# Optimization experiments

Hardware: AMD Instinct MI355X
Metric: run time of the kernel (lower is better)

The kernel has to match this reference:

```python
import jax, jax.numpy as jnp
import numpy as np

B, S, H, I, E, K = 2, 1024, 768, 1536, 8, 2
CAPACITY_FACTOR = 1.5
ROUTING_TEMP = 1.0
LB_WEIGHT = 0.001


def setup_inputs() -> dict:
    key = jax.random.key(0)
    k_x, k_g, k_w1, k_w3, k_w2 = jax.random.split(key, 5)
    std = 0.02
    return {
        "x": jax.random.normal(k_x, (B, S, H), dtype=jnp.float32),
        "w_gate": jax.random.normal(k_g, (H, E), dtype=jnp.float32) * 0.02,
        "w1": jax.random.normal(k_w1, (E, H, I), dtype=jnp.float32) * std,
        "w3": jax.random.normal(k_w3, (E, H, I), dtype=jnp.float32) * std,
        "w2": jax.random.normal(k_w2, (E, I, H), dtype=jnp.float32) * (std / np.sqrt(2 * 12)),
    }


def _moe_forward(x, w_gate, w1, w3, w2):
    Bb, Ss, Hh = x.shape
    T = Bb * Ss
    xf = x.reshape(T, Hh)

    # --- routing ---
    gate_logits = (xf @ w_gate) / ROUTING_TEMP          # [T, E]
    gate_probs = jax.nn.softmax(gate_logits, axis=-1)   # [T, E]
    topk_probs, topk_idx = jax.lax.top_k(gate_probs, K)  # [T, K]
    topk_probs = topk_probs / (topk_probs.sum(-1, keepdims=True) + 1e-8)

    # --- capacity dropping (per-k slot, token order, like the torch loop) ---
    capacity = max(8, int((T * K // E) * CAPACITY_FACTOR))
    onehot = (topk_idx[:, :, None] == jnp.arange(E)[None, None, :])  # [T, K, E] bool
    ranks = jnp.cumsum(onehot.astype(jnp.int32), axis=0)             # position of token in expert queue
    keep = onehot & (ranks <= capacity)                               # [T, K, E]

    # combine weight per (token, expert): sum over k of kept, clamped routing prob
    w_clamped = jnp.clip(topk_probs, 1e-8, 10.0)                      # [T, K]
    combine = jnp.einsum("tk,tke->te", w_clamped, keep.astype(xf.dtype))  # [T, E]

    # --- dense per-expert SwiGLU (reference form of masked dispatch) ---
    g = jnp.einsum("th,ehi->tei", xf, w1)   # [T, E, I]
    u = jnp.einsum("th,ehi->tei", xf, w3)   # [T, E, I]
    h = jax.nn.silu(g) * u                    # [T, E, I]
    y = jnp.einsum("tei,eih->teh", h, w2)   # [T, E, H]
    out = jnp.einsum("te,teh->th", combine, y).reshape(Bb, Ss, Hh)

    # --- load balancing loss ---
    expert_counts = keep.sum(axis=(0, 1)).astype(jnp.float32)         # [E]
    dropped = (onehot.sum() - keep.sum()).astype(jnp.float32)
    expert_usage = jax.lax.stop_gradient(expert_counts) / float(max(T * K, 1))
    gate_importance = gate_probs.mean(axis=0)                          # [E]
    aux = jnp.sum(expert_usage * gate_importance) * E
    aux = aux + jnp.where(dropped > 0, dropped / float(max(T, 1)) * 0.1, 0.0)
    aux = jnp.minimum(aux, 1.0) * LB_WEIGHT
    return out, aux


def reference(x, w_gate, w1, w3, w2):
    return _moe_forward(x, w_gate, w1, w3, w2)
```

## Files before the change

### kernel.cpp

```cpp
#include <hip/hip_runtime.h>
#include <math.h>

#define T_TOK 2048
#define HD 768
#define ID 1536
#define NE 8
#define CAP 768
#define TK 4096
#define MAXTILES 40

typedef __bf16 bf16_t;
typedef __bf16 bf16x8 __attribute__((ext_vector_type(8)));
typedef float floatx4 __attribute__((ext_vector_type(4)));

__device__ __forceinline__ void gld16(const bf16_t* g, bf16_t* l) {
  __builtin_amdgcn_global_load_lds(
      (__attribute__((address_space(1))) void*)(g),
      (__attribute__((address_space(3))) void*)(l),
      16, 0, 0);
}

__global__ void k_cvt_x(const float* __restrict__ x, bf16_t* __restrict__ xbf,
                        float* __restrict__ imp) {
  int i = blockIdx.x * 256 + threadIdx.x;
  if (blockIdx.x == 0 && threadIdx.x < NE) imp[threadIdx.x] = 0.f;
  const float4* xs = (const float4*)x;
  float4 a = xs[i * 2], b = xs[i * 2 + 1];
  bf16x8 v;
  v[0] = (bf16_t)a.x; v[1] = (bf16_t)a.y; v[2] = (bf16_t)a.z; v[3] = (bf16_t)a.w;
  v[4] = (bf16_t)b.x; v[5] = (bf16_t)b.y; v[6] = (bf16_t)b.z; v[7] = (bf16_t)b.w;
  *(bf16x8*)(xbf + (size_t)i * 8) = v;
}

__global__ void k_route(const float* __restrict__ x, const float* __restrict__ wg,
                        int2* __restrict__ idx2, float2* __restrict__ wc2,
                        float* __restrict__ imp) {
  int t = blockIdx.x;
  int lane = threadIdx.x;
  const float* xr = x + (size_t)t * HD;
  float acc[8] = {0, 0, 0, 0, 0, 0, 0, 0};
  for (int j = 0; j < 12; ++j) {
    int h = j * 64 + lane;
    float xv = xr[h];
    const float4* wr = (const float4*)(wg + (size_t)h * 8);
    float4 w0 = wr[0], w1 = wr[1];
    acc[0] += xv * w0.x; acc[1] += xv * w0.y; acc[2] += xv * w0.z; acc[3] += xv * w0.w;
    acc[4] += xv * w1.x; acc[5] += xv * w1.y; acc[6] += xv * w1.z; acc[7] += xv * w1.w;
  }
#pragma unroll
  for (int e = 0; e < 8; ++e) {
    float v = acc[e];
    for (int s = 1; s < 64; s <<= 1) v += __shfl_xor(v, s, 64);
    acc[e] = v;
  }
  float mx = acc[0];
#pragma unroll
  for (int e = 1; e < 8; ++e) mx = fmaxf(mx, acc[e]);
  float p[8], sum = 0.f;
#pragma unroll
  for (int e = 0; e < 8; ++e) { p[e] = __expf(acc[e] - mx); sum += p[e]; }
#pragma unroll
  for (int e = 0; e < 8; ++e) p[e] /= sum;
  if (lane < 8) atomicAdd(&imp[lane], p[lane]);
  if (lane == 0) {
    int e0 = 0;
#pragma unroll
    for (int e = 1; e < 8; ++e) if (p[e] > p[e0]) e0 = e;
    int e1 = (e0 == 0) ? 1 : 0;
#pragma unroll
    for (int e = 0; e < 8; ++e) if (e != e0 && p[e] > p[e1]) e1 = e;
    float denom = p[e0] + p[e1] + 1e-8f;
    float w0c = fminf(fmaxf(p[e0] / denom, 1e-8f), 10.f);
    float w1c = fminf(fmaxf(p[e1] / denom, 1e-8f), 10.f);
    idx2[t] = make_int2(e0, e1);
    wc2[t] = make_float2(w0c, w1c);
  }
}

__global__ void k_scan(const int2* __restrict__ idx2, const float2* __restrict__ wc2,
                       const float* __restrict__ imp,
                       int* __restrict__ tok_of_row, float* __restrict__ wgt_of_row,
                       int2* __restrict__ tok_rows, int4* __restrict__ tiles,
                       int* __restrict__ meta, float* __restrict__ aux_out) {
  __shared__ int sA[256][16];
  __shared__ int sB[256][8];
  __shared__ int tot8[8];
  int tid = threadIdx.x;
  int t0 = tid * 8;
#pragma unroll
  for (int c = 0; c < 16; ++c) sA[tid][c] = 0;
#pragma unroll
  for (int c = 0; c < 8; ++c) sB[tid][c] = 0;
  for (int j = 0; j < 8; ++j) {
    int t = t0 + j;
    int2 e2 = idx2[t];
    sA[tid][e2.x]++;
    sA[tid][8 + e2.y]++;
    tok_rows[t] = make_int2(-1, -1);
  }
  __syncthreads();
  for (int s = 1; s < 256; s <<= 1) {
    int v[16];
    if (tid >= s) {
#pragma unroll
      for (int c = 0; c < 16; ++c) v[c] = sA[tid - s][c];
    }
    __syncthreads();
    if (tid >= s) {
#pragma unroll
      for (int c = 0; c < 16; ++c) sA[tid][c] += v[c];
    }
    __syncthreads();
  }
  {
    int v[16];
#pragma unroll
    for (int c = 0; c < 16; ++c) v[c] = (tid > 0) ? sA[tid - 1][c] : 0;
    __syncthreads();
#pragma unroll
    for (int c = 0; c < 16; ++c) sA[tid][c] = v[c];
    __syncthreads();
  }
  int keepmask = 0;
  for (int j = 0; j < 8; ++j) {
    int t = t0 + j;
    int2 e2 = idx2[t];
    int r0 = ++sA[tid][e2.x];
    if (r0 <= CAP) { keepmask |= 1 << (j * 2); sB[tid][e2.x]++; }
    int r1 = ++sA[tid][8 + e2.y];
    if (r1 <= CAP) { keepmask |= 1 << (j * 2 + 1); sB[tid][e2.y]++; }
  }
  __syncthreads();
  for (int s = 1; s < 256; s <<= 1) {
    int v[8];
    if (tid >= s) {
#pragma unroll
      for (int c = 0; c < 8; ++c) v[c] = sB[tid - s][c];
    }
    __syncthreads();
    if (tid >= s) {
#pragma unroll
      for (int c = 0; c < 8; ++c) sB[tid][c] += v[c];
    }
    __syncthreads();
  }
  if (tid == 255) {
#pragma unroll
    for (int c = 0; c < 8; ++c) tot8[c] = sB[255][c];
  }
  __syncthreads();
  {
    int v[8];
#pragma unroll
    for (int c = 0; c < 8; ++c) v[c] = (tid > 0) ? sB[tid - 1][c] : 0;
    __syncthreads();
#pragma unroll
    for (int c = 0; c < 8; ++c) sB[tid][c] = v[c];
    __syncthreads();
  }
  int start8[8];
  {
    int run = 0;
#pragma unroll
    for (int c = 0; c < 8; ++c) { start8[c] = run; run += tot8[c]; }
  }
  for (int j = 0; j < 8; ++j) {
    int t = t0 + j;
    int2 e2 = idx2[t];
    float2 wv = wc2[t];
    if (keepmask & (1 << (j * 2))) {
      int pos = sB[tid][e2.x]++;
      int grow = start8[e2.x] + pos;
      tok_of_row[grow] = t; wgt_of_row[grow] = wv.x;
      tok_rows[t].x = grow;
    }
    if (keepmask & (1 << (j * 2 + 1))) {
      int pos = sB[tid][e2.y]++;
      int grow = start8[e2.y] + pos;
      tok_of_row[grow] = t; wgt_of_row[grow] = wv.y;
      tok_rows[t].y = grow;
    }
  }
  __syncthreads();
  if (tid == 0) {
    int numt = 0, totk = 0;
    for (int e = 0; e < NE; ++e) {
      int n = tot8[e]; totk += n; int s = start8[e];
      for (int j = 0; j < n; j += 128) tiles[numt++] = make_int4(e, s + j, min(128, n - j), 0);
    }
    meta[0] = numt;
    int dropped = TK - totk;
    float a = 0.f;
    for (int e = 0; e < NE; ++e)
      a += ((float)tot8[e] / (float)TK) * (imp[e] / (float)T_TOK);
    a *= (float)NE;
    if (dropped > 0) a += (float)dropped / (float)T_TOK * 0.1f;
    a = fminf(a, 1.f) * 0.001f;
    aux_out[0] = a;
  }
}

__global__ void k_tr(const float* __restrict__ src, bf16_t* __restrict__ dst,
                     int R, int C) {
  __shared__ bf16_t tl[64][65];
  int e = blockIdx.z;
  int r0 = blockIdx.y * 64, c0 = blockIdx.x * 64;
  int tid = threadIdx.x;
  int lr = tid >> 2, lc = (tid & 3) * 16;
  const float* s = src + ((size_t)e * R + (r0 + lr)) * C + c0 + lc;
#pragma unroll
  for (int j = 0; j < 16; j += 4) {
    float4 v = *(const float4*)(s + j);
    tl[lr][lc + j + 0] = (bf16_t)v.x;
    tl[lr][lc + j + 1] = (bf16_t)v.y;
    tl[lr][lc + j + 2] = (bf16_t)v.z;
    tl[lr][lc + j + 3] = (bf16_t)v.w;
  }
  __syncthreads();
  int oc = tid >> 2, orr = (tid & 3) * 16;
  bf16_t* d = dst + ((size_t)e * C + (c0 + oc)) * R + r0 + orr;
  bf16x8 v0, v1;
#pragma unroll
  for (int j = 0; j < 8; ++j) v0[j] = tl[orr + j][oc];
#pragma unroll
  for (int j = 0; j < 8; ++j) v1[j] = tl[orr + 8 + j][oc];
  *(bf16x8*)d = v0;
  *(bf16x8*)(d + 8) = v1;
}

__global__ __launch_bounds__(256, 2)
void k_gemm1(const bf16_t* __restrict__ xbf, const bf16_t* __restrict__ w1t,
             const bf16_t* __restrict__ w3t, const int* __restrict__ tok_of_row,
             const int4* __restrict__ tiles, const int* __restrict__ meta,
             bf16_t* __restrict__ h_ws) {
  int numt = meta[0];
  int bx = blockIdx.x;
  if (bx >= numt) return;
  int4 tlr = tiles[bx];
  int e = tlr.x, grow0 = tlr.y, nrows = tlr.z;
  int cy = blockIdx.y;

  __shared__ __attribute__((aligned(16))) bf16_t Abuf[128 * 32];
  __shared__ __attribute__((aligned(16))) bf16_t B1buf[128 * 32];
  __shared__ __attribute__((aligned(16))) bf16_t B3buf[128 * 32];

  int tid = threadIdx.x;
  int lane = tid & 63, wv = tid >> 6;
  int wm = wv & 1, wn = wv >> 1;
  int lr = lane & 15, q = lane >> 4;
  int rdc = (q ^ ((lane >> 1) & 3)) * 8;
  int srow = lane >> 2;
  int gch = ((lane & 3) ^ ((lane >> 3) & 3)) * 8;

  int ra = wv * 32 + srow;
  int tokA0 = tok_of_row[grow0 + min(ra, nrows - 1)];
  int tokA1 = tok_of_row[grow0 + min(ra + 16, nrows - 1)];
  const bf16_t* gA0 = xbf + (size_t)tokA0 * HD + gch;
  const bf16_t* gA1 = xbf + (size_t)tokA1 * HD + gch;
  int nb = cy * 128 + wv * 32 + srow;
  const bf16_t* gB1a = w1t + ((size_t)e * ID + nb) * HD + gch;
  const bf16_t* gB1b = gB1a + (size_t)16 * HD;
  const bf16_t* gB3a = w3t + ((size_t)e * ID + nb) * HD + gch;
  const bf16_t* gB3b = gB3a + (size_t)16 * HD;
  bf16_t* lA0 = &Abuf[(wv * 32) * 32];
  bf16_t* lA1 = &Abuf[(wv * 32 + 16) * 32];
  bf16_t* lB1a = &B1buf[(wv * 32) * 32];
  bf16_t* lB1b = &B1buf[(wv * 32 + 16) * 32];
  bf16_t* lB3a = &B3buf[(wv * 32) * 32];
  bf16_t* lB3b = &B3buf[(wv * 32 + 16) * 32];

  floatx4 accg[4][4] = {};
  floatx4 accu[4][4] = {};

  for (int kk = 0; kk < 24; ++kk) {
    __syncthreads();
    gld16(gA0, lA0);  gld16(gA1, lA1);
    gld16(gB1a, lB1a); gld16(gB1b, lB1b);
    gld16(gB3a, lB3a); gld16(gB3b, lB3b);
    gA0 += 32; gA1 += 32; gB1a += 32; gB1b += 32; gB3a += 32; gB3b += 32;
    __syncthreads();
    bf16x8 af[4], b1f[4], b3f[4];
#pragma unroll
    for (int i = 0; i < 4; ++i) af[i] = *(const bf16x8*)&Abuf[(wm * 64 + i * 16 + lr) * 32 + rdc];
#pragma unroll
    for (int i = 0; i < 4; ++i) b1f[i] = *(const bf16x8*)&B1buf[(wn * 64 + i * 16 + lr) * 32 + rdc];
#pragma unroll
    for (int i = 0; i < 4; ++i) b3f[i] = *(const bf16x8*)&B3buf[(wn * 64 + i * 16 + lr) * 32 + rdc];
#pragma unroll
    for (int i = 0; i < 4; ++i)
#pragma unroll
      for (int j = 0; j < 4; ++j) {
        accg[i][j] = __builtin_amdgcn_mfma_f32_16x16x32_bf16(af[i], b1f[j], accg[i][j], 0, 0, 0);
        accu[i][j] = __builtin_amdgcn_mfma_f32_16x16x32_bf16(af[i], b3f[j], accu[i][j], 0, 0, 0);
      }
  }
#pragma unroll
  for (int i = 0; i < 4; ++i)
#pragma unroll
    for (int r = 0; r < 4; ++r) {
      int rl = wm * 64 + i * 16 + q * 4 + r;
      if (rl < nrows) {
        size_t rb = (size_t)(grow0 + rl) * ID + cy * 128 + wn * 64 + lr;
#pragma unroll
        for (int j = 0; j < 4; ++j) {
          float gg = accg[i][j][r], uu = accu[i][j][r];
          float sg = gg / (1.f + __expf(-gg));
          h_ws[rb + j * 16] = (bf16_t)(sg * uu);
        }
      }
    }
}

__global__ __launch_bounds__(256, 2)
void k_gemm2(const bf16_t* __restrict__ h_ws, const bf16_t* __restrict__ w2t,
             const int4* __restrict__ tiles, const int* __restrict__ meta,
             float* __restrict__ y_ws) {
  int numt = meta[0];
  int bx = blockIdx.x;
  if (bx >= numt) return;
  int4 tlr = tiles[bx];
  int e = tlr.x, grow0 = tlr.y, nrows = tlr.z;
  int cy = blockIdx.y;

  __shared__ __attribute__((aligned(16))) bf16_t Abuf[128 * 32];
  __shared__ __attribute__((aligned(16))) bf16_t Bbuf[128 * 32];

  int tid = threadIdx.x;
  int lane = tid & 63, wv = tid >> 6;
  int wm = wv & 1, wn = wv >> 1;
  int lr = lane & 15, q = lane >> 4;
  int rdc = (q ^ ((lane >> 1) & 3)) * 8;
  int srow = lane >> 2;
  int gch = ((lane & 3) ^ ((lane >> 3) & 3)) * 8;

  int ra = wv * 32 + srow;
  const bf16_t* gA0 = h_ws + (size_t)(grow0 + min(ra, nrows - 1)) * ID + gch;
  const bf16_t* gA1 = h_ws + (size_t)(grow0 + min(ra + 16, nrows - 1)) * ID + gch;
  int nb = cy * 128 + wv * 32 + srow;
  const bf16_t* gB0 = w2t + ((size_t)e * HD + nb) * ID + gch;
  const bf16_t* gB1 = gB0 + (size_t)16 * ID;
  bf16_t* lA0 = &Abuf[(wv * 32) * 32];
  bf16_t* lA1 = &Abuf[(wv * 32 + 16) * 32];
  bf16_t* lB0 = &Bbuf[(wv * 32) * 32];
  bf16_t* lB1 = &Bbuf[(wv * 32 + 16) * 32];

  floatx4 acc[4][4] = {};

  for (int kk = 0; kk < 48; ++kk) {
    __syncthreads();
    gld16(gA0, lA0); gld16(gA1, lA1);
    gld16(gB0, lB0); gld16(gB1, lB1);
    gA0 += 32; gA1 += 32; gB0 += 32; gB1 += 32;
    __syncthreads();
    bf16x8 af[4], bfr[4];
#pragma unroll
    for (int i = 0; i < 4; ++i) af[i] = *(const bf16x8*)&Abuf[(wm * 64 + i * 16 + lr) * 32 + rdc];
#pragma unroll
    for (int i = 0; i < 4; ++i) bfr[i] = *(const bf16x8*)&Bbuf[(wn * 64 + i * 16 + lr) * 32 + rdc];
#pragma unroll
    for (int i = 0; i < 4; ++i)
#pragma unroll
      for (int j = 0; j < 4; ++j)
        acc[i][j] = __builtin_amdgcn_mfma_f32_16x16x32_bf16(af[i], bfr[j], acc[i][j], 0, 0, 0);
  }
#pragma unroll
  for (int i = 0; i < 4; ++i)
#pragma unroll
    for (int r = 0; r < 4; ++r) {
      int rl = wm * 64 + i * 16 + q * 4 + r;
      if (rl < nrows) {
        size_t rb = (size_t)(grow0 + rl) * HD + cy * 128 + wn * 64 + lr;
#pragma unroll
        for (int j = 0; j < 4; ++j) y_ws[rb + j * 16] = acc[i][j][r];
      }
    }
}

__global__ void k_comb(const float* __restrict__ y_ws, const int2* __restrict__ tok_rows,
                       const float* __restrict__ wgt_of_row, float* __restrict__ out) {
  int idx = blockIdx.x * 256 + threadIdx.x;
  int t = idx / 192;
  int c = idx - t * 192;
  int2 rr = tok_rows[t];
  float vx = 0.f, vy = 0.f, vz = 0.f, vw = 0.f;
  if (rr.x >= 0) {
    float w = wgt_of_row[rr.x];
    float4 a = *(const float4*)(y_ws + (size_t)rr.x * HD + c * 4);
    vx += w * a.x; vy += w * a.y; vz += w * a.z; vw += w * a.w;
  }
  if (rr.y >= 0) {
    float w = wgt_of_row[rr.y];
    float4 a = *(const float4*)(y_ws + (size_t)rr.y * HD + c * 4);
    vx += w * a.x; vy += w * a.y; vz += w * a.z; vw += w * a.w;
  }
  float4 v = make_float4(vx, vy, vz, vw);
  *(float4*)(out + (size_t)t * HD + c * 4) = v;
}

extern "C" void kernel_launch(void* const* d_in, const int* in_sizes, int n_in,
                              void* d_out, int out_size, void* d_ws, size_t ws_size,
                              hipStream_t stream) {
  const float* x  = (const float*)d_in[0];
  const float* wg = (const float*)d_in[1];
  const float* w1 = (const float*)d_in[2];
  const float* w3 = (const float*)d_in[3];
  const float* w2 = (const float*)d_in[4];
  float* out = (float*)d_out;

  char* ws = (char*)d_ws;
  bf16_t* xbf  = (bf16_t*)(ws + 0);
  bf16_t* w1t  = (bf16_t*)(ws + 3145728);
  bf16_t* w3t  = (bf16_t*)(ws + 22020096);
  bf16_t* w2t  = (bf16_t*)(ws + 40894464);
  bf16_t* h_ws = (bf16_t*)(ws + 59768832);
  float*  y_ws = (float*)(ws + 72351744);
  int2*   idx2 = (int2*)(ws + 84934656);
  float2* wc2  = (float2*)(ws + 84951040);
  int*    tok_of_row = (int*)(ws + 84967424);
  float*  wgt_of_row = (float*)(ws + 84983808);
  int2*   tok_rows   = (int2*)(ws + 85000192);
  int4*   tiles      = (int4*)(ws + 85016576);
  int*    meta       = (int*)(ws + 85017600);
  float*  imp        = (float*)(ws + 85017856);

  float* aux_out = out + (size_t)T_TOK * HD;

  k_cvt_x<<<768, 256, 0, stream>>>(x, xbf, imp);
  k_route<<<T_TOK, 64, 0, stream>>>(x, wg, idx2, wc2, imp);
  k_scan<<<1, 256, 0, stream>>>(idx2, wc2, imp, tok_of_row, wgt_of_row,
                                tok_rows, tiles, meta, aux_out);
  k_tr<<<dim3(24, 12, 8), 256, 0, stream>>>(w1, w1t, HD, ID);
  k_tr<<<dim3(24, 12, 8), 256, 0, stream>>>(w3, w3t, HD, ID);
  k_tr<<<dim3(12, 24, 8), 256, 0, stream>>>(w2, w2t, ID, HD);
  k_gemm1<<<dim3(MAXTILES, 12), 256, 0, stream>>>(xbf, w1t, w3t, tok_of_row,
                                                  tiles, meta, h_ws);
  k_gemm2<<<dim3(MAXTILES, 6), 256, 0, stream>>>(h_ws, w2t, tiles, meta, y_ws);
  k_comb<<<1536, 256, 0, stream>>>(y_ws, tok_rows, wgt_of_row, out);
}
```

Measured before the change: 285.6 us.

## Fuse routing/convert, simplify scan, merge transposes, shrink GEMM tiles, atomic combine

Folds the x-to-bf16 conversion into the routing kernel and replaces the two-pass per-thread prefix scan with a warp-shuffle scan per (slot, expert) wave. The three weight transpose launches become one, and the tile list is replaced by a fixed per-expert grid. Both GEMMs narrow their N tile from 128 to 64 with higher occupancy hints to launch more blocks. The combine kernel and the y workspace are removed: gemm2 scales its results and atomically adds them into a zeroed output. This cuts launches and a round trip through global memory, at the cost of float atomics, nondeterministic summation order and more A-tile reloads.

```diff
diff --git a/kernel.cpp b/kernel.cpp
--- a/kernel.cpp
+++ b/kernel.cpp
@@ -7,10 +7,10 @@
 #define NE 8
 #define CAP 768
 #define TK 4096
-#define MAXTILES 40
 
 typedef __bf16 bf16_t;
 typedef __bf16 bf16x8 __attribute__((ext_vector_type(8)));
+typedef __bf16 bf16x4 __attribute__((ext_vector_type(4)));
 typedef float floatx4 __attribute__((ext_vector_type(4)));
 
 __device__ __forceinline__ void gld16(const bf16_t* g, bf16_t* l) {
@@ -20,32 +20,32 @@
       16, 0, 0);
 }
 
-__global__ void k_cvt_x(const float* __restrict__ x, bf16_t* __restrict__ xbf,
+__global__ void k_route(const float* __restrict__ x, const float* __restrict__ wg,
+                        bf16_t* __restrict__ xbf, int2* __restrict__ idx2,
+                        float2* __restrict__ wc2, int2* __restrict__ tok_rows,
                         float* __restrict__ imp) {
-  int i = blockIdx.x * 256 + threadIdx.x;
-  if (blockIdx.x == 0 && threadIdx.x < NE) imp[threadIdx.x] = 0.f;
-  const float4* xs = (const float4*)x;
-  float4 a = xs[i * 2], b = xs[i * 2 + 1];
-  bf16x8 v;
-  v[0] = (bf16_t)a.x; v[1] = (bf16_t)a.y; v[2] = (bf16_t)a.z; v[3] = (bf16_t)a.w;
-  v[4] = (bf16_t)b.x; v[5] = (bf16_t)b.y; v[6] = (bf16_t)b.z; v[7] = (bf16_t)b.w;
-  *(bf16x8*)(xbf + (size_t)i * 8) = v;
-}
-
-__global__ void k_route(const float* __restrict__ x, const float* __restrict__ wg,
-                        int2* __restrict__ idx2, float2* __restrict__ wc2,
-                        float* __restrict__ imp) {
-  int t = blockIdx.x;
-  int lane = threadIdx.x;
+  int t = blockIdx.x * 4 + (threadIdx.x >> 6);
+  int lane = threadIdx.x & 63;
   const float* xr = x + (size_t)t * HD;
+  int off = lane * 12;
+  float4 a = *(const float4*)(xr + off);
+  float4 b = *(const float4*)(xr + off + 4);
+  float4 c = *(const float4*)(xr + off + 8);
+  float xv[12] = {a.x, a.y, a.z, a.w, b.x, b.y, b.z, b.w, c.x, c.y, c.z, c.w};
+  bf16x4 s0, s1, s2;
+#pragma unroll
+  for (int j = 0; j < 4; ++j) { s0[j] = (bf16_t)xv[j]; s1[j] = (bf16_t)xv[4 + j]; s2[j] = (bf16_t)xv[8 + j]; }
+  bf16_t* xo = xbf + (size_t)t * HD + off;
+  *(bf16x4*)xo = s0; *(bf16x4*)(xo + 4) = s1; *(bf16x4*)(xo + 8) = s2;
+
   float acc[8] = {0, 0, 0, 0, 0, 0, 0, 0};
-  for (int j = 0; j < 12; ++j) {
-    int h = j * 64 + lane;
-    float xv = xr[h];
-    const float4* wr = (const float4*)(wg + (size_t)h * 8);
+#pragma unroll
+  for (int jj = 0; jj < 12; ++jj) {
+    const float4* wr = (const float4*)(wg + (size_t)(off + jj) * 8);
     float4 w0 = wr[0], w1 = wr[1];
-    acc[0] += xv * w0.x; acc[1] += xv * w0.y; acc[2] += xv * w0.z; acc[3] += xv * w0.w;
-    acc[4] += xv * w1.x; acc[5] += xv * w1.y; acc[6] += xv * w1.z; acc[7] += xv * w1.w;
+    float v = xv[jj];
+    acc[0] += v * w0.x; acc[1] += v * w0.y; acc[2] += v * w0.z; acc[3] += v * w0.w;
+    acc[4] += v * w1.x; acc[5] += v * w1.y; acc[6] += v * w1.z; acc[7] += v * w1.w;
   }
 #pragma unroll
   for (int e = 0; e < 8; ++e) {
@@ -74,143 +74,92 @@
     float w1c = fminf(fmaxf(p[e1] / denom, 1e-8f), 10.f);
     idx2[t] = make_int2(e0, e1);
     wc2[t] = make_float2(w0c, w1c);
+    tok_rows[t] = make_int2(-1, -1);
   }
 }
 
 __global__ void k_scan(const int2* __restrict__ idx2, const float2* __restrict__ wc2,
                        const float* __restrict__ imp,
                        int* __restrict__ tok_of_row, float* __restrict__ wgt_of_row,
-                       int2* __restrict__ tok_rows, int4* __restrict__ tiles,
-                       int* __restrict__ meta, float* __restrict__ aux_out) {
-  __shared__ int sA[256][16];
-  __shared__ int sB[256][8];
-  __shared__ int tot8[8];
+                       int2* __restrict__ tok_rows, int2* __restrict__ cnt_start,
+                       float* __restrict__ aux_out) {
+  __shared__ int sTot[16];
+  __shared__ int sPos[8];
   int tid = threadIdx.x;
-  int t0 = tid * 8;
-#pragma unroll
-  for (int c = 0; c < 16; ++c) sA[tid][c] = 0;
-#pragma unroll
-  for (int c = 0; c < 8; ++c) sB[tid][c] = 0;
-  for (int j = 0; j < 8; ++j) {
-    int t = t0 + j;
-    int2 e2 = idx2[t];
-    sA[tid][e2.x]++;
-    sA[tid][8 + e2.y]++;
-    tok_rows[t] = make_int2(-1, -1);
-  }
-  __syncthreads();
-  for (int s = 1; s < 256; s <<= 1) {
-    int v[16];
-    if (tid >= s) {
-#pragma unroll
-      for (int c = 0; c < 16; ++c) v[c] = sA[tid - s][c];
-    }
-    __syncthreads();
-    if (tid >= s) {
-#pragma unroll
-      for (int c = 0; c < 16; ++c) sA[tid][c] += v[c];
-    }
-    __syncthreads();
-  }
-  {
-    int v[16];
-#pragma unroll
-    for (int c = 0; c < 16; ++c) v[c] = (tid > 0) ? sA[tid - 1][c] : 0;
-    __syncthreads();
-#pragma unroll
-    for (int c = 0; c < 16; ++c) sA[tid][c] = v[c];
-    __syncthreads();
-  }
-  int keepmask = 0;
-  for (int j = 0; j < 8; ++j) {
-    int t = t0 + j;
-    int2 e2 = idx2[t];
-    int r0 = ++sA[tid][e2.x];
-    if (r0 <= CAP) { keepmask |= 1 << (j * 2); sB[tid][e2.x]++; }
-    int r1 = ++sA[tid][8 + e2.y];
-    if (r1 <= CAP) { keepmask |= 1 << (j * 2 + 1); sB[tid][e2.y]++; }
-  }
-  __syncthreads();
-  for (int s = 1; s < 256; s <<= 1) {
-    int v[8];
-    if (tid >= s) {
-#pragma unroll
-      for (int c = 0; c < 8; ++c) v[c] = sB[tid - s][c];
-    }
-    __syncthreads();
-    if (tid >= s) {
-#pragma unroll
-      for (int c = 0; c < 8; ++c) sB[tid][c] += v[c];
-    }
-    __syncthreads();
-  }
-  if (tid == 255) {
-#pragma unroll
-    for (int c = 0; c < 8; ++c) tot8[c] = sB[255][c];
-  }
-  __syncthreads();
-  {
-    int v[8];
-#pragma unroll
-    for (int c = 0; c < 8; ++c) v[c] = (tid > 0) ? sB[tid - 1][c] : 0;
-    __syncthreads();
-#pragma unroll
-    for (int c = 0; c < 8; ++c) sB[tid][c] = v[c];
-    __syncthreads();
-  }
-  int start8[8];
-  {
-    int run = 0;
-#pragma unroll
-    for (int c = 0; c < 8; ++c) { start8[c] = run; run += tot8[c]; }
-  }
-  for (int j = 0; j < 8; ++j) {
-    int t = t0 + j;
-    int2 e2 = idx2[t];
-    float2 wv = wc2[t];
-    if (keepmask & (1 << (j * 2))) {
-      int pos = sB[tid][e2.x]++;
-      int grow = start8[e2.x] + pos;
-      tok_of_row[grow] = t; wgt_of_row[grow] = wv.x;
-      tok_rows[t].x = grow;
-    }
-    if (keepmask & (1 << (j * 2 + 1))) {
-      int pos = sB[tid][e2.y]++;
-      int grow = start8[e2.y] + pos;
-      tok_of_row[grow] = t; wgt_of_row[grow] = wv.y;
-      tok_rows[t].y = grow;
-    }
-  }
+  int w = tid >> 6, lane = tid & 63;
+  int s = w >> 3, e = w & 7;
+  int t0 = lane * 32;
+  int cnt = 0;
+  for (int j = 0; j < 32; ++j) {
+    int2 p = idx2[t0 + j];
+    int ex = s ? p.y : p.x;
+    cnt += (ex == e) ? 1 : 0;
+  }
+  int incl = cnt;
+  for (int d = 1; d < 64; d <<= 1) {
+    int v = __shfl_up(incl, d, 64);
+    if (lane >= d) incl += v;
+  }
+  int excl = incl - cnt;
+  if (lane == 63) sTot[w] = incl;
   __syncthreads();
   if (tid == 0) {
-    int numt = 0, totk = 0;
-    for (int e = 0; e < NE; ++e) {
-      int n = tot8[e]; totk += n; int s = start8[e];
-      for (int j = 0; j < n; j += 128) tiles[numt++] = make_int4(e, s + j, min(128, n - j), 0);
+    int run = 0;
+    float a = 0.f;
+    for (int ee = 0; ee < 8; ++ee) {
+      int k = min(sTot[ee], CAP) + min(sTot[8 + ee], CAP);
+      sPos[ee] = run;
+      cnt_start[ee] = make_int2(run, k);
+      a += ((float)k / (float)TK) * (imp[ee] / (float)T_TOK);
+      run += k;
     }
-    meta[0] = numt;
-    int dropped = TK - totk;
-    float a = 0.f;
-    for (int e = 0; e < NE; ++e)
-      a += ((float)tot8[e] / (float)TK) * (imp[e] / (float)T_TOK);
     a *= (float)NE;
+    int dropped = TK - run;
     if (dropped > 0) a += (float)dropped / (float)T_TOK * 0.1f;
     a = fminf(a, 1.f) * 0.001f;
     aux_out[0] = a;
   }
-}
-
-__global__ void k_tr(const float* __restrict__ src, bf16_t* __restrict__ dst,
-                     int R, int C) {
+  __syncthreads();
+  int rank = excl;
+  for (int j = 0; j < 32; ++j) {
+    int t = t0 + j;
+    int2 p = idx2[t];
+    int ex = s ? p.y : p.x;
+    if (ex == e) {
+      rank++;
+      if (rank <= CAP) {
+        int pos = atomicAdd(&sPos[e], 1);
+        tok_of_row[pos] = t;
+        float2 wv = wc2[t];
+        wgt_of_row[pos] = s ? wv.y : wv.x;
+        ((int*)tok_rows)[2 * t + s] = pos;
+      }
+    }
+  }
+}
+
+__global__ void k_tr(const float* __restrict__ w1, const float* __restrict__ w3,
+                     const float* __restrict__ w2, bf16_t* __restrict__ w1t,
+                     bf16_t* __restrict__ w3t, bf16_t* __restrict__ w2t) {
   __shared__ bf16_t tl[64][65];
-  int e = blockIdx.z;
-  int r0 = blockIdx.y * 64, c0 = blockIdx.x * 64;
+  int z = blockIdx.z;
+  const float* src; bf16_t* dst; int R, C, r0, c0;
+  if (z < 16) {
+    R = HD; C = ID; r0 = blockIdx.y * 64; c0 = blockIdx.x * 64;
+    int e = z & 7;
+    if (z < 8) { src = w1 + (size_t)e * R * C; dst = w1t + (size_t)e * R * C; }
+    else       { src = w3 + (size_t)e * R * C; dst = w3t + (size_t)e * R * C; }
+  } else {
+    R = ID; C = HD; r0 = blockIdx.x * 64; c0 = blockIdx.y * 64;
+    int e = z - 16;
+    src = w2 + (size_t)e * R * C; dst = w2t + (size_t)e * R * C;
+  }
   int tid = threadIdx.x;
   int lr = tid >> 2, lc = (tid & 3) * 16;
-  const float* s = src + ((size_t)e * R + (r0 + lr)) * C + c0 + lc;
+  const float* sp = src + (size_t)(r0 + lr) * C + c0 + lc;
 #pragma unroll
   for (int j = 0; j < 16; j += 4) {
-    float4 v = *(const float4*)(s + j);
+    float4 v = *(const float4*)(sp + j);
     tl[lr][lc + j + 0] = (bf16_t)v.x;
     tl[lr][lc + j + 1] = (bf16_t)v.y;
     tl[lr][lc + j + 2] = (bf16_t)v.z;
@@ -218,7 +167,7 @@
   }
   __syncthreads();
   int oc = tid >> 2, orr = (tid & 3) * 16;
-  bf16_t* d = dst + ((size_t)e * C + (c0 + oc)) * R + r0 + orr;
+  bf16_t* d = dst + (size_t)(c0 + oc) * R + r0 + orr;
   bf16x8 v0, v1;
 #pragma unroll
   for (int j = 0; j < 8; ++j) v0[j] = tl[orr + j][oc];
@@ -228,21 +177,21 @@
   *(bf16x8*)(d + 8) = v1;
 }
 
-__global__ __launch_bounds__(256, 2)
+__global__ __launch_bounds__(256, 3)
 void k_gemm1(const bf16_t* __restrict__ xbf, const bf16_t* __restrict__ w1t,
              const bf16_t* __restrict__ w3t, const int* __restrict__ tok_of_row,
-             const int4* __restrict__ tiles, const int* __restrict__ meta,
-             bf16_t* __restrict__ h_ws) {
-  int numt = meta[0];
-  int bx = blockIdx.x;
-  if (bx >= numt) return;
-  int4 tlr = tiles[bx];
-  int e = tlr.x, grow0 = tlr.y, nrows = tlr.z;
+             const int2* __restrict__ cnt_start, bf16_t* __restrict__ h_ws) {
+  int e = blockIdx.x & 7, j = blockIdx.x >> 3;
+  int2 cs = cnt_start[e];
+  int nrows = cs.y - j * 128;
+  if (nrows <= 0) return;
+  if (nrows > 128) nrows = 128;
+  int grow0 = cs.x + j * 128;
   int cy = blockIdx.y;
 
   __shared__ __attribute__((aligned(16))) bf16_t Abuf[128 * 32];
-  __shared__ __attribute__((aligned(16))) bf16_t B1buf[128 * 32];
-  __shared__ __attribute__((aligned(16))) bf16_t B3buf[128 * 32];
+  __shared__ __attribute__((aligned(16))) bf16_t B1buf[64 * 32];
+  __shared__ __attribute__((aligned(16))) bf16_t B3buf[64 * 32];
 
   int tid = threadIdx.x;
   int lane = tid & 63, wv = tid >> 6;
@@ -257,41 +206,36 @@
   int tokA1 = tok_of_row[grow0 + min(ra + 16, nrows - 1)];
   const bf16_t* gA0 = xbf + (size_t)tokA0 * HD + gch;
   const bf16_t* gA1 = xbf + (size_t)tokA1 * HD + gch;
-  int nb = cy * 128 + wv * 32 + srow;
-  const bf16_t* gB1a = w1t + ((size_t)e * ID + nb) * HD + gch;
-  const bf16_t* gB1b = gB1a + (size_t)16 * HD;
-  const bf16_t* gB3a = w3t + ((size_t)e * ID + nb) * HD + gch;
-  const bf16_t* gB3b = gB3a + (size_t)16 * HD;
+  int nb = cy * 64 + wv * 16 + srow;
+  const bf16_t* gB1 = w1t + ((size_t)e * ID + nb) * HD + gch;
+  const bf16_t* gB3 = w3t + ((size_t)e * ID + nb) * HD + gch;
   bf16_t* lA0 = &Abuf[(wv * 32) * 32];
   bf16_t* lA1 = &Abuf[(wv * 32 + 16) * 32];
-  bf16_t* lB1a = &B1buf[(wv * 32) * 32];
-  bf16_t* lB1b = &B1buf[(wv * 32 + 16) * 32];
-  bf16_t* lB3a = &B3buf[(wv * 32) * 32];
-  bf16_t* lB3b = &B3buf[(wv * 32 + 16) * 32];
-
-  floatx4 accg[4][4] = {};
-  floatx4 accu[4][4] = {};
+  bf16_t* lB1 = &B1buf[(wv * 16) * 32];
+  bf16_t* lB3 = &B3buf[(wv * 16) * 32];
+
+  floatx4 accg[4][2] = {};
+  floatx4 accu[4][2] = {};
 
   for (int kk = 0; kk < 24; ++kk) {
     __syncthreads();
-    gld16(gA0, lA0);  gld16(gA1, lA1);
-    gld16(gB1a, lB1a); gld16(gB1b, lB1b);
-    gld16(gB3a, lB3a); gld16(gB3b, lB3b);
-    gA0 += 32; gA1 += 32; gB1a += 32; gB1b += 32; gB3a += 32; gB3b += 32;
+    gld16(gA0, lA0); gld16(gA1, lA1);
+    gld16(gB1, lB1); gld16(gB3, lB3);
+    gA0 += 32; gA1 += 32; gB1 += 32; gB3 += 32;
     __syncthreads();
-    bf16x8 af[4], b1f[4], b3f[4];
+    bf16x8 af[4], b1f[2], b3f[2];
 #pragma unroll
     for (int i = 0; i < 4; ++i) af[i] = *(const bf16x8*)&Abuf[(wm * 64 + i * 16 + lr) * 32 + rdc];
 #pragma unroll
-    for (int i = 0; i < 4; ++i) b1f[i] = *(const bf16x8*)&B1buf[(wn * 64 + i * 16 + lr) * 32 + rdc];
-#pragma unroll
-    for (int i = 0; i < 4; ++i) b3f[i] = *(const bf16x8*)&B3buf[(wn * 64 + i * 16 + lr) * 32 + rdc];
+    for (int i = 0; i < 2; ++i) b1f[i] = *(const bf16x8*)&B1buf[(wn * 32 + i * 16 + lr) * 32 + rdc];
+#pragma unroll
+    for (int i = 0; i < 2; ++i) b3f[i] = *(const bf16x8*)&B3buf[(wn * 32 + i * 16 + lr) * 32 + rdc];
 #pragma unroll
     for (int i = 0; i < 4; ++i)
 #pragma unroll
-      for (int j = 0; j < 4; ++j) {
-        accg[i][j] = __builtin_amdgcn_mfma_f32_16x16x32_bf16(af[i], b1f[j], accg[i][j], 0, 0, 0);
-        accu[i][j] = __builtin_amdgcn_mfma_f32_16x16x32_bf16(af[i], b3f[j], accu[i][j], 0, 0, 0);
+      for (int jj = 0; jj < 2; ++jj) {
+        accg[i][jj] = __builtin_amdgcn_mfma_f32_16x16x32_bf16(af[i], b1f[jj], accg[i][jj], 0, 0, 0);
+        accu[i][jj] = __builtin_amdgcn_mfma_f32_16x16x32_bf16(af[i], b3f[jj], accu[i][jj], 0, 0, 0);
       }
   }
 #pragma unroll
@@ -300,30 +244,31 @@
     for (int r = 0; r < 4; ++r) {
       int rl = wm * 64 + i * 16 + q * 4 + r;
       if (rl < nrows) {
-        size_t rb = (size_t)(grow0 + rl) * ID + cy * 128 + wn * 64 + lr;
-#pragma unroll
-        for (int j = 0; j < 4; ++j) {
-          float gg = accg[i][j][r], uu = accu[i][j][r];
+        size_t rb = (size_t)(grow0 + rl) * ID + cy * 64 + wn * 32 + lr;
+#pragma unroll
+        for (int jj = 0; jj < 2; ++jj) {
+          float gg = accg[i][jj][r], uu = accu[i][jj][r];
           float sg = gg / (1.f + __expf(-gg));
-          h_ws[rb + j * 16] = (bf16_t)(sg * uu);
+          h_ws[rb + jj * 16] = (bf16_t)(sg * uu);
         }
       }
     }
 }
 
-__global__ __launch_bounds__(256, 2)
+__global__ __launch_bounds__(256, 4)
 void k_gemm2(const bf16_t* __restrict__ h_ws, const bf16_t* __restrict__ w2t,
-             const int4* __restrict__ tiles, const int* __restrict__ meta,
-             float* __restrict__ y_ws) {
-  int numt = meta[0];
-  int bx = blockIdx.x;
-  if (bx >= numt) return;
-  int4 tlr = tiles[bx];
-  int e = tlr.x, grow0 = tlr.y, nrows = tlr.z;
+             const int* __restrict__ tok_of_row, const float* __restrict__ wgt_of_row,
+             const int2* __restrict__ cnt_start, float* __restrict__ out) {
+  int e = blockIdx.x & 7, j = blockIdx.x >> 3;
+  int2 cs = cnt_start[e];
+  int nrows = cs.y - j * 128;
+  if (nrows <= 0) return;
+  if (nrows > 128) nrows = 128;
+  int grow0 = cs.x + j * 128;
   int cy = blockIdx.y;
 
   __shared__ __attribute__((aligned(16))) bf16_t Abuf[128 * 32];
-  __shared__ __attribute__((aligned(16))) bf16_t Bbuf[128 * 32];
+  __shared__ __attribute__((aligned(16))) bf16_t Bbuf[64 * 32];
 
   int tid = threadIdx.x;
   int lane = tid & 63, wv = tid >> 6;
@@ -336,32 +281,30 @@
   int ra = wv * 32 + srow;
   const bf16_t* gA0 = h_ws + (size_t)(grow0 + min(ra, nrows - 1)) * ID + gch;
   const bf16_t* gA1 = h_ws + (size_t)(grow0 + min(ra + 16, nrows - 1)) * ID + gch;
-  int nb = cy * 128 + wv * 32 + srow;
-  const bf16_t* gB0 = w2t + ((size_t)e * HD + nb) * ID + gch;
-  const bf16_t* gB1 = gB0 + (size_t)16 * ID;
+  int nb = cy * 64 + wv * 16 + srow;
+  const bf16_t* gB = w2t + ((size_t)e * HD + nb) * ID + gch;
   bf16_t* lA0 = &Abuf[(wv * 32) * 32];
   bf16_t* lA1 = &Abuf[(wv * 32 + 16) * 32];
-  bf16_t* lB0 = &Bbuf[(wv * 32) * 32];
-  bf16_t* lB1 = &Bbuf[(wv * 32 + 16) * 32];
-
-  floatx4 acc[4][4] = {};
+  bf16_t* lB = &Bbuf[(wv * 16) * 32];
+
+  floatx4 acc[4][2] = {};
 
   for (int kk = 0; kk < 48; ++kk) {
     __syncthreads();
     gld16(gA0, lA0); gld16(gA1, lA1);
-    gld16(gB0, lB0); gld16(gB1, lB1);
-    gA0 += 32; gA1 += 32; gB0 += 32; gB1 += 32;
+    gld16(gB, lB);
+    gA0 += 32; gA1 += 32; gB += 32;
     __syncthreads();
-    bf16x8 af[4], bfr[4];
+    bf16x8 af[4], bfr[2];
 #pragma unroll
     for (int i = 0; i < 4; ++i) af[i] = *(const bf16x8*)&Abuf[(wm * 64 + i * 16 + lr) * 32 + rdc];
 #pragma unroll
-    for (int i = 0; i < 4; ++i) bfr[i] = *(const bf16x8*)&Bbuf[(wn * 64 + i * 16 + lr) * 32 + rdc];
+    for (int i = 0; i < 2; ++i) bfr[i] = *(const bf16x8*)&Bbuf[(wn * 32 + i * 16 + lr) * 32 + rdc];
 #pragma unroll
     for (int i = 0; i < 4; ++i)
 #pragma unroll
-      for (int j = 0; j < 4; ++j)
-        acc[i][j] = __builtin_amdgcn_mfma_f32_16x16x32_bf16(af[i], bfr[j], acc[i][j], 0, 0, 0);
+      for (int jj = 0; jj < 2; ++jj)
+        acc[i][jj] = __builtin_amdgcn_mfma_f32_16x16x32_bf16(af[i], bfr[jj], acc[i][jj], 0, 0, 0);
   }
 #pragma unroll
   for (int i = 0; i < 4; ++i)
@@ -369,32 +312,15 @@
     for (int r = 0; r < 4; ++r) {
       int rl = wm * 64 + i * 16 + q * 4 + r;
       if (rl < nrows) {
-        size_t rb = (size_t)(grow0 + rl) * HD + cy * 128 + wn * 64 + lr;
-#pragma unroll
-        for (int j = 0; j < 4; ++j) y_ws[rb + j * 16] = acc[i][j][r];
+        int grow = grow0 + rl;
+        int tok = tok_of_row[grow];
+        float wgt = wgt_of_row[grow];
+        size_t ob = (size_t)tok * HD + cy * 64 + wn * 32 + lr;
+#pragma unroll
+        for (int jj = 0; jj < 2; ++jj)
+          atomicAdd(&out[ob + jj * 16], wgt * acc[i][jj][r]);
       }
     }
-}
-
-__global__ void k_comb(const float* __restrict__ y_ws, const int2* __restrict__ tok_rows,
-                       const float* __restrict__ wgt_of_row, float* __restrict__ out) {
-  int idx = blockIdx.x * 256 + threadIdx.x;
-  int t = idx / 192;
-  int c = idx - t * 192;
-  int2 rr = tok_rows[t];
-  float vx = 0.f, vy = 0.f, vz = 0.f, vw = 0.f;
-  if (rr.x >= 0) {
-    float w = wgt_of_row[rr.x];
-    float4 a = *(const float4*)(y_ws + (size_t)rr.x * HD + c * 4);
-    vx += w * a.x; vy += w * a.y; vz += w * a.z; vw += w * a.w;
-  }
-  if (rr.y >= 0) {
-    float w = wgt_of_row[rr.y];
-    float4 a = *(const float4*)(y_ws + (size_t)rr.y * HD + c * 4);
-    vx += w * a.x; vy += w * a.y; vz += w * a.z; vw += w * a.w;
-  }
-  float4 v = make_float4(vx, vy, vz, vw);
-  *(float4*)(out + (size_t)t * HD + c * 4) = v;
 }
 
 extern "C" void kernel_launch(void* const* d_in, const int* in_sizes, int n_in,
@@ -413,27 +339,24 @@
   bf16_t* w3t  = (bf16_t*)(ws + 22020096);
   bf16_t* w2t  = (bf16_t*)(ws + 40894464);
   bf16_t* h_ws = (bf16_t*)(ws + 59768832);
-  float*  y_ws = (float*)(ws + 72351744);
-  int2*   idx2 = (int2*)(ws + 84934656);
-  float2* wc2  = (float2*)(ws + 84951040);
-  int*    tok_of_row = (int*)(ws + 84967424);
-  float*  wgt_of_row = (float*)(ws + 84983808);
-  int2*   tok_rows   = (int2*)(ws + 85000192);
-  int4*   tiles      = (int4*)(ws + 85016576);
-  int*    meta       = (int*)(ws + 85017600);
-  float*  imp        = (float*)(ws + 85017856);
+  int2*   idx2 = (int2*)(ws + 72351744);
+  float2* wc2  = (float2*)(ws + 72368128);
+  int*    tok_of_row = (int*)(ws + 72384512);
+  float*  wgt_of_row = (float*)(ws + 72400896);
+  int2*   tok_rows   = (int2*)(ws + 72417280);
+  int2*   cnt_start  = (int2*)(ws + 72433664);
+  float*  imp        = (float*)(ws + 72433728);
 
   float* aux_out = out + (size_t)T_TOK * HD;
 
-  k_cvt_x<<<768, 256, 0, stream>>>(x, xbf, imp);
-  k_route<<<T_TOK, 64, 0, stream>>>(x, wg, idx2, wc2, imp);
-  k_scan<<<1, 256, 0, stream>>>(idx2, wc2, imp, tok_of_row, wgt_of_row,
-                                tok_rows, tiles, meta, aux_out);
-  k_tr<<<dim3(24, 12, 8), 256, 0, stream>>>(w1, w1t, HD, ID);
-  k_tr<<<dim3(24, 12, 8), 256, 0, stream>>>(w3, w3t, HD, ID);
-  k_tr<<<dim3(12, 24, 8), 256, 0, stream>>>(w2, w2t, ID, HD);
-  k_gemm1<<<dim3(MAXTILES, 12), 256, 0, stream>>>(xbf, w1t, w3t, tok_of_row,
-                                                  tiles, meta, h_ws);
-  k_gemm2<<<dim3(MAXTILES, 6), 256, 0, stream>>>(h_ws, w2t, tiles, meta, y_ws);
-  k_comb<<<1536, 256, 0, stream>>>(y_ws, tok_rows, wgt_of_row, out);
-}
+  hipMemsetAsync(out, 0, (size_t)T_TOK * HD * sizeof(float), stream);
+  hipMemsetAsync(imp, 0, NE * sizeof(float), stream);
+  k_route<<<512, 256, 0, stream>>>(x, wg, xbf, idx2, wc2, tok_rows, imp);
+  k_scan<<<1, 1024, 0, stream>>>(idx2, wc2, imp, tok_of_row, wgt_of_row,
+                                 tok_rows, cnt_start, aux_out);
+  k_tr<<<dim3(24, 12, 24), 256, 0, stream>>>(w1, w3, w2, w1t, w3t, w2t);
+  k_gemm1<<<dim3(96, 24), 256, 0, stream>>>(xbf, w1t, w3t, tok_of_row,
+                                            cnt_start, h_ws);
+  k_gemm2<<<dim3(96, 12), 256, 0, stream>>>(h_ws, w2t, tok_of_row, wgt_of_row,
+                                            cnt_start, out);
+}
```

Result: no change. 288.7 us (+1.1%).
